# Kernel tuning notes

Measured on AMD Instinct MI355X. Metric: run time of the kernel, lower is better.

Reference implementation:

```python
import jax, jax.numpy as jnp
import numpy as np

IN, H, T = 1024, 2048, 2048

def setup_inputs() -> dict:
    key = jax.random.key(0)
    ks = jax.random.split(key, 10)
    x = jax.random.normal(ks[0], (1, T, IN), dtype=jnp.float32)
    # strictly increasing timestamps
    time = jnp.cumsum(jax.random.uniform(ks[1], (T,), dtype=jnp.float32))
    # xavier-ish scaled weights, uniform(0,1) biases as in init_weights
    W_ih = jax.random.normal(ks[2], (4 * H, IN), dtype=jnp.float32) * (1.0 / np.sqrt(IN))
    W_hh = jax.random.normal(ks[3], (4 * H, H), dtype=jnp.float32) * (1.0 / np.sqrt(H))
    b_ih = jax.random.uniform(ks[4], (4 * H,), dtype=jnp.float32)
    b_hh = jax.random.uniform(ks[5], (4 * H,), dtype=jnp.float32)
    decay_w = jax.random.normal(ks[6], (H,), dtype=jnp.float32)
    decay_b = jax.random.uniform(ks[7], (H,), dtype=jnp.float32)
    h0 = jax.random.normal(ks[8], (1, H), dtype=jnp.float32) * 0.1
    c0 = jax.random.normal(ks[9], (1, H), dtype=jnp.float32) * 0.1
    return {"x": x, "time": time, "W_ih": W_ih, "W_hh": W_hh, "b_ih": b_ih,
            "b_hh": b_hh, "decay_w": decay_w, "decay_b": decay_b, "h0": h0, "c0": c0}


def reference(x, time, W_ih, W_hh, b_ih, b_hh, decay_w, decay_b, h0, c0):
    Tn = x.shape[1]
    Hn = h0.shape[1]
    # dt[i] = time[i] - time[i-1], dt[0] = 0
    dt = jnp.concatenate([jnp.zeros((1,), x.dtype), time[1:] - time[:-1]])
    # step i (i>0) decays h with gamma(dt[i-1]); step 0 uses gamma = 1
    dt_prev = jnp.concatenate([jnp.zeros((1,), x.dtype), dt[:-1]])  # [T]
    gamma = jnp.exp(-jax.nn.relu(dt_prev[:, None] * decay_w[None, :] + decay_b[None, :]))  # [T,H]
    gamma = jnp.where((jnp.arange(Tn) > 0)[:, None], gamma, jnp.ones((), x.dtype))
    # precompute input contribution for all steps: [T, 4H]
    xg = x[0] @ W_ih.T + b_ih + b_hh

    def step(carry, inp):
        h, c = carry  # [H], [H]
        xg_t, gamma_t = inp
        h = h * gamma_t
        gates = xg_t + h @ W_hh.T  # [4H]
        i_, f_, g_, o_ = jnp.split(gates, 4)
        i_ = jax.nn.sigmoid(i_)
        f_ = jax.nn.sigmoid(f_)
        g_ = jnp.tanh(g_)
        o_ = jax.nn.sigmoid(o_)
        c = f_ * c + i_ * g_
        h = o_ * jnp.tanh(c)
        return (h, c), h

    (h_f, c_f), hs = jax.lax.scan(step, (h0[0], c0[0]), (xg, gamma))  # hs: [T,H]
    # dot-product attention pooling against final hidden state
    attn = hs @ h_f  # [T]
    w = jax.nn.softmax(attn)
    context = w @ hs  # [H]
    return context[None, :]  # [1, H]
```

## Files before the change

kernel.cpp:

```cpp
#include <hip/hip_runtime.h>
#include <hip/hip_bf16.h>

#define H 2048
#define T 2048
#define INPUT 1024
#define FOURH 8192
#define NBLK 256
#define RING 512

typedef __attribute__((ext_vector_type(8))) short bf16x8;
typedef __attribute__((ext_vector_type(4))) float f32x4_t;

__device__ __forceinline__ unsigned short f2bf(float f) {
  union { float f; unsigned u; } v; v.f = f;
  unsigned r = v.u + 0x7FFFu + ((v.u >> 16) & 1u);
  return (unsigned short)(r >> 16);
}

__device__ __forceinline__ float fast_tanh(float x) {
  float e = __expf(fminf(-2.f * x, 80.f));
  return (1.f - e) / (1.f + e);
}

__global__ void prep_kernel(const float* __restrict__ x, const float* __restrict__ W_ih,
                            const float* __restrict__ time_, short* __restrict__ xb,
                            short* __restrict__ wb, float* __restrict__ dtp,
                            unsigned* __restrict__ flags) {
  size_t i = (size_t)blockIdx.x * blockDim.x + threadIdx.x;
  size_t stride = (size_t)gridDim.x * blockDim.x;
  if (i < (size_t)T * INPUT) xb[i] = (short)f2bf(x[i]);
  for (size_t j = i; j < (size_t)FOURH * INPUT; j += stride) wb[j] = (short)f2bf(W_ih[j]);
  if (i < T) dtp[i] = (i >= 2) ? (time_[i - 1] - time_[i - 2]) : 0.0f;
  if (i < NBLK) flags[i] = 0u;
}

__global__ void __launch_bounds__(256)
gemm_xg(const short* __restrict__ A, const short* __restrict__ B,
        const float* __restrict__ b_ih, const float* __restrict__ b_hh,
        float* __restrict__ xg) {
  int wave = threadIdx.x >> 6;
  int lane = threadIdx.x & 63;
  int bid = blockIdx.x;
  int m0 = (bid & 15) << 7;
  int n0 = ((bid >> 4) << 6) + (wave << 4);
  int r16 = lane & 15, q = lane >> 4;
  const short* ap = A + (size_t)(m0 + r16) * INPUT + q * 8;
  const short* bp = B + (size_t)(n0 + r16) * INPUT + q * 8;
  f32x4_t acc[8];
#pragma unroll
  for (int s = 0; s < 8; ++s) acc[s] = {0.f, 0.f, 0.f, 0.f};
  for (int k = 0; k < INPUT; k += 32) {
    bf16x8 bv = *(const bf16x8*)(bp + k);
#pragma unroll
    for (int s = 0; s < 8; ++s) {
      bf16x8 av = *(const bf16x8*)(ap + (size_t)(s << 4) * INPUT + k);
      acc[s] = __builtin_amdgcn_mfma_f32_16x16x32_bf16(av, bv, acc[s], 0, 0, 0);
    }
  }
  int n = n0 + r16;
  float bias = b_ih[n] + b_hh[n];
#pragma unroll
  for (int s = 0; s < 8; ++s) {
#pragma unroll
    for (int r = 0; r < 4; ++r) {
      int m = m0 + (s << 4) + q * 4 + r;
      xg[(size_t)m * FOURH + n] = acc[s][r] + bias;
    }
  }
}

__device__ __forceinline__ void epoch_bar(unsigned* flags, unsigned e) {
  __syncthreads();
  if (threadIdx.x == 0)
    __hip_atomic_store(&flags[blockIdx.x], e, __ATOMIC_RELEASE, __HIP_MEMORY_SCOPE_AGENT);
  if (threadIdx.x < NBLK) {
    while (__hip_atomic_load(&flags[threadIdx.x], __ATOMIC_RELAXED,
                             __HIP_MEMORY_SCOPE_AGENT) < e) {
    }
  }
  __builtin_amdgcn_fence(__ATOMIC_ACQUIRE, "agent");
  __syncthreads();
}

__global__ void __launch_bounds__(512, 2)
lstm_rec(const float* __restrict__ xg, const float* __restrict__ W_hh,
         const float* __restrict__ decay_w, const float* __restrict__ decay_b,
         const float* __restrict__ h0, const float* __restrict__ c0,
         const float* __restrict__ dtp, float* __restrict__ hs,
         unsigned long long* ring, unsigned* flags) {
  const int wave = threadIdx.x >> 6;
  const int lane = threadIdx.x & 63;
  const int u = (blockIdx.x << 3) + wave;
  __shared__ __align__(16) float lh[H];

  float wreg[4][32];
#pragma unroll
  for (int g = 0; g < 4; ++g) {
    const float* wr = W_hh + (size_t)(g * H + u) * H + (lane << 2);
#pragma unroll
    for (int p = 0; p < 8; ++p)
      *(f32x4_t*)&wreg[g][p << 2] = *(const f32x4_t*)(wr + (p << 8));
  }
  const float dw = decay_w[u], db = decay_b[u];
  float c = c0[u];
  if (lane == 0) {
    union { float f; unsigned u; } hv; hv.f = h0[u];
    __hip_atomic_store(&ring[u], (1ull << 32) | hv.u, __ATOMIC_RELAXED,
                       __HIP_MEMORY_SCOPE_AGENT);
  }

  for (int t = 0; t < T; ++t) {
    if ((t & 255) == 0 && t) epoch_bar(flags, (unsigned)(t >> 8));

    float xv = 0.f, gam = 0.f;
    if (lane < 4) xv = xg[(size_t)t * FOURH + (size_t)lane * H + u];
    if (lane == 0 && t + 1 < T) gam = __expf(-fmaxf(0.f, dtp[t + 1] * dw + db));

    const unsigned want = (unsigned)t + 1u;
    unsigned long long* sp =
        ring + (((size_t)(t & (RING - 1)) << 11) | (unsigned)((wave << 8) + lane));
    unsigned long long w0, w1, w2, w3;
    for (;;) {
      w0 = __hip_atomic_load(sp,       __ATOMIC_RELAXED, __HIP_MEMORY_SCOPE_AGENT);
      w1 = __hip_atomic_load(sp + 64,  __ATOMIC_RELAXED, __HIP_MEMORY_SCOPE_AGENT);
      w2 = __hip_atomic_load(sp + 128, __ATOMIC_RELAXED, __HIP_MEMORY_SCOPE_AGENT);
      w3 = __hip_atomic_load(sp + 192, __ATOMIC_RELAXED, __HIP_MEMORY_SCOPE_AGENT);
      int bad = ((unsigned)(w0 >> 32) != want) | ((unsigned)(w1 >> 32) != want) |
                ((unsigned)(w2 >> 32) != want) | ((unsigned)(w3 >> 32) != want);
      if (!__any(bad)) break;
    }
    {
      float* lw = lh + (wave << 8) + lane;
      union { unsigned u; float f; } v;
      v.u = (unsigned)w0; lw[0]   = v.f;
      v.u = (unsigned)w1; lw[64]  = v.f;
      v.u = (unsigned)w2; lw[128] = v.f;
      v.u = (unsigned)w3; lw[192] = v.f;
    }
    __syncthreads();

    float a0 = 0.f, a1 = 0.f, a2 = 0.f, a3 = 0.f;
#pragma unroll
    for (int p = 0; p < 8; ++p) {
      f32x4_t h4 = *(const f32x4_t*)(lh + (p << 8) + (lane << 2));
#pragma unroll
      for (int e = 0; e < 4; ++e) {
        float h = h4[e];
        a0 += wreg[0][(p << 2) + e] * h;
        a1 += wreg[1][(p << 2) + e] * h;
        a2 += wreg[2][(p << 2) + e] * h;
        a3 += wreg[3][(p << 2) + e] * h;
      }
    }
#pragma unroll
    for (int s = 32; s >= 1; s >>= 1) {
      a0 += __shfl_xor(a0, s);
      a1 += __shfl_xor(a1, s);
      a2 += __shfl_xor(a2, s);
      a3 += __shfl_xor(a3, s);
    }

    {
      float pre = ((lane == 0) ? a0 : (lane == 1) ? a1 : (lane == 2) ? a2 : a3) + xv;
      float ps = (lane == 2) ? 2.f * pre : pre;
      float sg = 1.f / (1.f + __expf(-ps));
      float act = (lane == 2) ? 2.f * sg - 1.f : sg;
      float iv = __shfl(act, 0), fv = __shfl(act, 1), gv = __shfl(act, 2),
            ov = __shfl(act, 3);
      c = fv * c + iv * gv;
      float h = ov * fast_tanh(c);
      if (lane == 0 && t + 1 < T) {
        union { float f; unsigned u; } hv; hv.f = h * gam;
        size_t slot = (size_t)((t + 1) & (RING - 1)) << 11;
        __hip_atomic_store(&ring[slot | (unsigned)u],
                           (((unsigned long long)(t + 2)) << 32) | hv.u,
                           __ATOMIC_RELAXED, __HIP_MEMORY_SCOPE_AGENT);
      }
      if (lane == 1) hs[(size_t)t * H + u] = h;
    }
    __syncthreads();
  }
}

__global__ void attn_k(const float* __restrict__ hs, float* __restrict__ attn) {
  int t = blockIdx.x;
  const float* row = hs + (size_t)t * H;
  const float* hf = hs + (size_t)(T - 1) * H;
  float s = 0.f;
  for (int i = threadIdx.x; i < H; i += 256) s += row[i] * hf[i];
#pragma unroll
  for (int o = 32; o; o >>= 1) s += __shfl_down(s, o);
  __shared__ float wsum[4];
  if ((threadIdx.x & 63) == 0) wsum[threadIdx.x >> 6] = s;
  __syncthreads();
  if (threadIdx.x == 0) attn[t] = wsum[0] + wsum[1] + wsum[2] + wsum[3];
}

__global__ void softmax_k(float* __restrict__ a) {
  int tid = threadIdx.x;
  __shared__ float red[16];
  __shared__ float bcast;
  float m = -1e30f;
  for (int i = tid; i < T; i += 1024) m = fmaxf(m, a[i]);
#pragma unroll
  for (int o = 32; o; o >>= 1) m = fmaxf(m, __shfl_xor(m, o));
  if ((tid & 63) == 0) red[tid >> 6] = m;
  __syncthreads();
  if (tid == 0) {
    float mm = red[0];
    for (int i = 1; i < 16; ++i) mm = fmaxf(mm, red[i]);
    bcast = mm;
  }
  __syncthreads();
  float M = bcast, s = 0.f;
  for (int i = tid; i < T; i += 1024) { float e = __expf(a[i] - M); a[i] = e; s += e; }
#pragma unroll
  for (int o = 32; o; o >>= 1) s += __shfl_xor(s, o);
  if ((tid & 63) == 0) red[tid >> 6] = s;
  __syncthreads();
  if (tid == 0) {
    float ss = 0.f;
    for (int i = 0; i < 16; ++i) ss += red[i];
    bcast = 1.f / ss;
  }
  __syncthreads();
  float inv = bcast;
  for (int i = tid; i < T; i += 1024) a[i] *= inv;
}

__global__ void ctx_k(const float* __restrict__ hs, const float* __restrict__ w,
                      float* __restrict__ out) {
  int h = (blockIdx.x << 8) + threadIdx.x;
  int t0 = blockIdx.y << 6;
  float acc = 0.f;
  for (int t = t0; t < t0 + 64; ++t) acc += w[t] * hs[(size_t)t * H + h];
  atomicAdd(&out[h], acc);
}

extern "C" void kernel_launch(void* const* d_in, const int* in_sizes, int n_in,
                              void* d_out, int out_size, void* d_ws, size_t ws_size,
                              hipStream_t stream) {
  const float* x       = (const float*)d_in[0];
  const float* time_   = (const float*)d_in[1];
  const float* W_ih    = (const float*)d_in[2];
  const float* W_hh    = (const float*)d_in[3];
  const float* b_ih    = (const float*)d_in[4];
  const float* b_hh    = (const float*)d_in[5];
  const float* decay_w = (const float*)d_in[6];
  const float* decay_b = (const float*)d_in[7];
  const float* h0      = (const float*)d_in[8];
  const float* c0      = (const float*)d_in[9];

  char* ws = (char*)d_ws;
  float*    xg   = (float*)ws;
  float*    hs   = (float*)(ws + (64u << 20));
  short*    xb   = (short*)(ws + (80u << 20));
  short*    wb   = (short*)(ws + (84u << 20));
  unsigned long long* ring = (unsigned long long*)(ws + (100u << 20));
  float*    dtp  = (float*)(ws + (108u << 20));
  float*    attn = dtp + T;
  unsigned* flags = (unsigned*)(attn + T);

  prep_kernel<<<8192, 256, 0, stream>>>(x, W_ih, time_, xb, wb, dtp, flags);

  gemm_xg<<<2048, 256, 0, stream>>>(xb, wb, b_ih, b_hh, xg);

  {
    void* args[] = {&xg, (void*)&W_hh, (void*)&decay_w, (void*)&decay_b,
                    (void*)&h0, (void*)&c0, &dtp, &hs, &ring, &flags};
    (void)hipLaunchCooperativeKernel((void*)lstm_rec, dim3(NBLK), dim3(512), args, 0, stream);
  }

  attn_k<<<T, 256, 0, stream>>>(hs, attn);
  softmax_k<<<1, 1024, 0, stream>>>(attn);
  (void)hipMemsetAsync(d_out, 0, out_size * sizeof(float), stream);
  ctx_k<<<dim3(H / 256, T / 64), 256, 0, stream>>>(hs, attn, (float*)d_out);
}
```

Baseline: 6.282 ms.

## Fuse attention pooling into recurrent kernel and double-buffer ring polling

The attention scores, softmax and context reduction now run as tail phases of the cooperative recurrent kernel, separated by grid-wide epoch barriers, which removes three extra kernel launches and one memset placed late in the stream. The ring-buffer spin-wait now alternates between two sets of in-flight loads, so a new poll is already issued while the previous one is checked, aiming to cut the handoff latency between steps. The cost is two extra grid barriers and more register pressure in an already register-heavy kernel. The per-step loop is the dominant cost, and the changes to it are small.

```diff
diff --git a/kernel.cpp b/kernel.cpp
--- a/kernel.cpp
+++ b/kernel.cpp
@@ -87,11 +87,13 @@
          const float* __restrict__ decay_w, const float* __restrict__ decay_b,
          const float* __restrict__ h0, const float* __restrict__ c0,
          const float* __restrict__ dtp, float* __restrict__ hs,
-         unsigned long long* ring, unsigned* flags) {
+         unsigned long long* ring, unsigned* flags, float* __restrict__ attn,
+         float* __restrict__ out) {
   const int wave = threadIdx.x >> 6;
   const int lane = threadIdx.x & 63;
   const int u = (blockIdx.x << 3) + wave;
   __shared__ __align__(16) float lh[H];
+  __shared__ float red[16];
 
   float wreg[4][32];
 #pragma unroll
@@ -109,6 +111,15 @@
                        __HIP_MEMORY_SCOPE_AGENT);
   }
 
+#define PISSUE(d0, d1, d2, d3)                                                         \
+  d0 = __hip_atomic_load(sp,       __ATOMIC_RELAXED, __HIP_MEMORY_SCOPE_AGENT);        \
+  d1 = __hip_atomic_load(sp + 64,  __ATOMIC_RELAXED, __HIP_MEMORY_SCOPE_AGENT);        \
+  d2 = __hip_atomic_load(sp + 128, __ATOMIC_RELAXED, __HIP_MEMORY_SCOPE_AGENT);        \
+  d3 = __hip_atomic_load(sp + 192, __ATOMIC_RELAXED, __HIP_MEMORY_SCOPE_AGENT);
+#define PTAGOK(d0, d1, d2, d3)                                                         \
+  (((unsigned)(d0 >> 32) == want) & ((unsigned)(d1 >> 32) == want) &                   \
+   ((unsigned)(d2 >> 32) == want) & ((unsigned)(d3 >> 32) == want))
+
   for (int t = 0; t < T; ++t) {
     if ((t & 255) == 0 && t) epoch_bar(flags, (unsigned)(t >> 8));
 
@@ -119,15 +130,15 @@
     const unsigned want = (unsigned)t + 1u;
     unsigned long long* sp =
         ring + (((size_t)(t & (RING - 1)) << 11) | (unsigned)((wave << 8) + lane));
-    unsigned long long w0, w1, w2, w3;
+    unsigned long long w0, w1, w2, w3, v0, v1, v2, v3;
+    PISSUE(w0, w1, w2, w3)
     for (;;) {
-      w0 = __hip_atomic_load(sp,       __ATOMIC_RELAXED, __HIP_MEMORY_SCOPE_AGENT);
-      w1 = __hip_atomic_load(sp + 64,  __ATOMIC_RELAXED, __HIP_MEMORY_SCOPE_AGENT);
-      w2 = __hip_atomic_load(sp + 128, __ATOMIC_RELAXED, __HIP_MEMORY_SCOPE_AGENT);
-      w3 = __hip_atomic_load(sp + 192, __ATOMIC_RELAXED, __HIP_MEMORY_SCOPE_AGENT);
-      int bad = ((unsigned)(w0 >> 32) != want) | ((unsigned)(w1 >> 32) != want) |
-                ((unsigned)(w2 >> 32) != want) | ((unsigned)(w3 >> 32) != want);
-      if (!__any(bad)) break;
+      PISSUE(v0, v1, v2, v3)
+      __builtin_amdgcn_sched_barrier(0);
+      if (__all(PTAGOK(w0, w1, w2, w3))) break;
+      PISSUE(w0, w1, w2, w3)
+      __builtin_amdgcn_sched_barrier(0);
+      if (__all(PTAGOK(v0, v1, v2, v3))) { w0 = v0; w1 = v1; w2 = v2; w3 = v3; break; }
     }
     {
       float* lw = lh + (wave << 8) + lane;
@@ -180,61 +191,70 @@
     }
     __syncthreads();
   }
-}
-
-__global__ void attn_k(const float* __restrict__ hs, float* __restrict__ attn) {
-  int t = blockIdx.x;
-  const float* row = hs + (size_t)t * H;
-  const float* hf = hs + (size_t)(T - 1) * H;
-  float s = 0.f;
-  for (int i = threadIdx.x; i < H; i += 256) s += row[i] * hf[i];
-#pragma unroll
-  for (int o = 32; o; o >>= 1) s += __shfl_down(s, o);
-  __shared__ float wsum[4];
-  if ((threadIdx.x & 63) == 0) wsum[threadIdx.x >> 6] = s;
-  __syncthreads();
-  if (threadIdx.x == 0) attn[t] = wsum[0] + wsum[1] + wsum[2] + wsum[3];
-}
-
-__global__ void softmax_k(float* __restrict__ a) {
-  int tid = threadIdx.x;
-  __shared__ float red[16];
-  __shared__ float bcast;
-  float m = -1e30f;
-  for (int i = tid; i < T; i += 1024) m = fmaxf(m, a[i]);
-#pragma unroll
-  for (int o = 32; o; o >>= 1) m = fmaxf(m, __shfl_xor(m, o));
-  if ((tid & 63) == 0) red[tid >> 6] = m;
-  __syncthreads();
-  if (tid == 0) {
-    float mm = red[0];
-    for (int i = 1; i < 16; ++i) mm = fmaxf(mm, red[i]);
-    bcast = mm;
-  }
-  __syncthreads();
-  float M = bcast, s = 0.f;
-  for (int i = tid; i < T; i += 1024) { float e = __expf(a[i] - M); a[i] = e; s += e; }
-#pragma unroll
-  for (int o = 32; o; o >>= 1) s += __shfl_xor(s, o);
-  if ((tid & 63) == 0) red[tid >> 6] = s;
-  __syncthreads();
-  if (tid == 0) {
-    float ss = 0.f;
-    for (int i = 0; i < 16; ++i) ss += red[i];
-    bcast = 1.f / ss;
-  }
-  __syncthreads();
-  float inv = bcast;
-  for (int i = tid; i < T; i += 1024) a[i] *= inv;
-}
-
-__global__ void ctx_k(const float* __restrict__ hs, const float* __restrict__ w,
-                      float* __restrict__ out) {
-  int h = (blockIdx.x << 8) + threadIdx.x;
-  int t0 = blockIdx.y << 6;
-  float acc = 0.f;
-  for (int t = t0; t < t0 + 64; ++t) acc += w[t] * hs[(size_t)t * H + h];
-  atomicAdd(&out[h], acc);
+#undef PISSUE
+#undef PTAGOK
+
+  epoch_bar(flags, 8);
+
+  {
+    const float* rowp = hs + (size_t)u * H;
+    const float* hfp = hs + (size_t)(T - 1) * H;
+    float s = 0.f;
+#pragma unroll
+    for (int p = 0; p < 8; ++p) {
+      f32x4_t rv = *(const f32x4_t*)(rowp + (p << 8) + (lane << 2));
+      f32x4_t fv = *(const f32x4_t*)(hfp + (p << 8) + (lane << 2));
+      s += rv[0] * fv[0] + rv[1] * fv[1] + rv[2] * fv[2] + rv[3] * fv[3];
+    }
+#pragma unroll
+    for (int o = 32; o; o >>= 1) s += __shfl_xor(s, o);
+    if (lane == 0) attn[u] = s;
+  }
+  epoch_bar(flags, 9);
+
+  if (blockIdx.x >= 64) return;
+
+  {
+    const int tid = threadIdx.x;
+    f32x4_t av = *(const f32x4_t*)(attn + (tid << 2));
+    float m = fmaxf(fmaxf(av[0], av[1]), fmaxf(av[2], av[3]));
+#pragma unroll
+    for (int o = 32; o; o >>= 1) m = fmaxf(m, __shfl_xor(m, o));
+    if (lane == 0) red[wave] = m;
+    __syncthreads();
+    float M = red[0];
+#pragma unroll
+    for (int i = 1; i < 8; ++i) M = fmaxf(M, red[i]);
+    float e0 = __expf(av[0] - M), e1 = __expf(av[1] - M), e2 = __expf(av[2] - M),
+          e3 = __expf(av[3] - M);
+    float s = e0 + e1 + e2 + e3;
+#pragma unroll
+    for (int o = 32; o; o >>= 1) s += __shfl_xor(s, o);
+    __syncthreads();
+    if (lane == 0) red[wave] = s;
+    __syncthreads();
+    float S = red[0] + red[1] + red[2] + red[3] + red[4] + red[5] + red[6] + red[7];
+    float inv = 1.f / S;
+    f32x4_t wv = {e0 * inv, e1 * inv, e2 * inv, e3 * inv};
+    *(f32x4_t*)(lh + (tid << 2)) = wv;
+    __syncthreads();
+
+    const int tB = blockIdx.x << 5;
+    const float* hp = hs + (size_t)tB * H + (tid << 2);
+    float ac0 = 0.f, ac1 = 0.f, ac2 = 0.f, ac3 = 0.f;
+#pragma unroll 4
+    for (int tt = 0; tt < 32; ++tt) {
+      float wt = lh[tB + tt];
+      f32x4_t hv = *(const f32x4_t*)hp;
+      hp += H;
+      ac0 += wt * hv[0]; ac1 += wt * hv[1]; ac2 += wt * hv[2]; ac3 += wt * hv[3];
+    }
+    int hbase = tid << 2;
+    atomicAdd(&out[hbase + 0], ac0);
+    atomicAdd(&out[hbase + 1], ac1);
+    atomicAdd(&out[hbase + 2], ac2);
+    atomicAdd(&out[hbase + 3], ac3);
+  }
 }
 
 extern "C" void kernel_launch(void* const* d_in, const int* in_sizes, int n_in,
@@ -260,19 +280,17 @@
   float*    dtp  = (float*)(ws + (108u << 20));
   float*    attn = dtp + T;
   unsigned* flags = (unsigned*)(attn + T);
+  float*    outp = (float*)d_out;
 
   prep_kernel<<<8192, 256, 0, stream>>>(x, W_ih, time_, xb, wb, dtp, flags);
 
   gemm_xg<<<2048, 256, 0, stream>>>(xb, wb, b_ih, b_hh, xg);
+
+  (void)hipMemsetAsync(d_out, 0, out_size * sizeof(float), stream);
 
   {
     void* args[] = {&xg, (void*)&W_hh, (void*)&decay_w, (void*)&decay_b,
-                    (void*)&h0, (void*)&c0, &dtp, &hs, &ring, &flags};
+                    (void*)&h0, (void*)&c0, &dtp, &hs, &ring, &flags, &attn, &outp};
     (void)hipLaunchCooperativeKernel((void*)lstm_rec, dim3(NBLK), dim3(512), args, 0, stream);
   }
-
-  attn_k<<<T, 256, 0, stream>>>(hs, attn);
-  softmax_k<<<1, 1024, 0, stream>>>(attn);
-  (void)hipMemsetAsync(d_out, 0, out_size * sizeof(float), stream);
-  ctx_k<<<dim3(H / 256, T / 64), 256, 0, stream>>>(hs, attn, (float*)d_out);
-}
+}
```

Result: slower. 7.205 ms (+14.7%).
